# Kernel optimization log

Hardware: AMD Instinct MI355X
Metric: run time of the kernel (lower is better)

Reference implementation:

```python
import jax, jax.numpy as jnp
import numpy as np

D_MODEL = 1536
D_STATE = 96
D_CONV = 4
EXPAND = 2
COND_DIM = 1536
D_INNER = D_MODEL * EXPAND
DT_RANK = max(D_MODEL // 16, 1)
EPS = 1e-6


def setup_inputs() -> dict:
    key = jax.random.key(0)
    ks = jax.random.split(key, 12)
    B, L = 2, 2048
    s = 0.02
    x = jax.random.normal(ks[0], (B, L, D_MODEL), dtype=jnp.float32)
    t_cond = jax.random.normal(ks[1], (B, 1, COND_DIM), dtype=jnp.float32)
    cond_w = s * jax.random.normal(ks[2], (COND_DIM, 3 * D_MODEL), dtype=jnp.float32)
    cond_b = jnp.zeros((3 * D_MODEL,), dtype=jnp.float32).at[2 * D_MODEL:].set(2.0)
    in_w = s * jax.random.normal(ks[3], (D_MODEL, 2 * D_INNER), dtype=jnp.float32)
    conv_w = s * jax.random.normal(ks[4], (D_INNER, 1, D_CONV), dtype=jnp.float32)  # depthwise [O,I/g,K]
    conv_b = s * jax.random.normal(ks[5], (D_INNER,), dtype=jnp.float32)
    xproj_w = s * jax.random.normal(ks[6], (D_INNER, DT_RANK + 2 * D_STATE), dtype=jnp.float32)
    dt_w = s * jax.random.normal(ks[7], (DT_RANK, D_INNER), dtype=jnp.float32)
    dt_b = s * jax.random.normal(ks[8], (D_INNER,), dtype=jnp.float32)
    A_log = jnp.log(jnp.broadcast_to(jnp.arange(1, D_STATE + 1, dtype=jnp.float32)[None, :], (D_INNER, D_STATE)))
    D_param = jnp.ones((D_INNER,), dtype=jnp.float32)
    out_w = s * jax.random.normal(ks[9], (D_INNER, D_MODEL), dtype=jnp.float32)
    return {"x": x, "t_cond": t_cond, "cond_w": cond_w, "cond_b": cond_b,
            "in_w": in_w, "conv_w": conv_w, "conv_b": conv_b, "xproj_w": xproj_w,
            "dt_w": dt_w, "dt_b": dt_b, "A_log": A_log, "D_param": D_param, "out_w": out_w}


def _forward(x, t_cond, cond_w, cond_b, in_w, conv_w, conv_b, xproj_w, dt_w, dt_b, A_log, D_param, out_w):
    residual = x
    B, L, _ = x.shape
    # AdaRMSNorm
    rms = jax.lax.rsqrt(jnp.mean(x * x, axis=-1, keepdims=True) + EPS)
    xn = x * rms
    cond = t_cond @ cond_w + cond_b  # [B,1,3*D_MODEL]
    scale, shift, gate = jnp.split(cond, 3, axis=-1)
    xm = jax.nn.sigmoid(gate) * (xn * (1.0 + scale) + shift)
    # in_proj and split
    xz = xm @ in_w  # [B,L,2*D_INNER]
    x_main, z = xz[..., :D_INNER], xz[..., D_INNER:]
    # causal depthwise conv1d (torch pads both sides then slices [:L] -> left pad only)
    xc = jnp.swapaxes(x_main, 1, 2)  # [B,D_INNER,L]
    xc = jax.lax.conv_general_dilated(xc, conv_w, window_strides=(1,),
                                      padding=[(D_CONV - 1, 0)],
                                      feature_group_count=D_INNER,
                                      dimension_numbers=("NCH", "OIH", "NCH"))
    xc = xc + conv_b[None, :, None]
    x_main = jax.nn.silu(jnp.swapaxes(xc, 1, 2))  # [B,L,D_INNER]
    # SSM parameters
    A = -jnp.exp(A_log)  # [D_INNER,D_STATE]
    x_dbl = x_main @ xproj_w
    dt_raw = x_dbl[..., :DT_RANK]
    B_ssm = x_dbl[..., DT_RANK:DT_RANK + D_STATE]
    C_ssm = x_dbl[..., DT_RANK + D_STATE:]
    dt = jax.nn.softplus(dt_raw @ dt_w + dt_b)  # [B,L,D_INNER]
    # selective scan over time (avoids materializing [B,L,D_INNER,D_STATE])
    def step(state, inp):
        dt_t, B_t, C_t, x_t = inp  # [B,Di],[B,Ds],[B,Ds],[B,Di]
        dA = jnp.exp(dt_t[:, :, None] * A)  # [B,Di,Ds]
        state = state * dA + (dt_t * x_t)[:, :, None] * B_t[:, None, :]
        y_t = jnp.einsum("bdn,bn->bd", state, C_t)
        return state, y_t

    state0 = jnp.zeros((B, D_INNER, D_STATE), dtype=x.dtype)
    xs = (jnp.swapaxes(dt, 0, 1), jnp.swapaxes(B_ssm, 0, 1),
          jnp.swapaxes(C_ssm, 0, 1), jnp.swapaxes(x_main, 0, 1))
    _, y = jax.lax.scan(step, state0, xs)  # y: [L,B,D_INNER]
    y = jnp.swapaxes(y, 0, 1)
    y = y + x_main * D_param[None, None, :]
    y = y * jax.nn.silu(z)
    return residual + y @ out_w


def reference(x, t_cond, cond_w, cond_b, in_w, conv_w, conv_b, xproj_w, dt_w, dt_b, A_log, D_param, out_w):
    return _forward(x, t_cond, cond_w, cond_b, in_w, conv_w, conv_b, xproj_w, dt_w, dt_b, A_log, D_param, out_w)
```

## Files before the change

### kernel.cpp

```cpp
#include <hip/hip_runtime.h>
#include <hip/hip_bf16.h>
#include <cstdint>
#include <cstddef>

#define L_SEQ 2048
#define NBATCH 2
#define M_TOT 4096
#define DM 1536
#define DI 3072
#define DS 96
#define DTR 96
#define XDBL_LD 384

typedef __attribute__((ext_vector_type(8))) short bf16x8;
typedef __attribute__((ext_vector_type(4))) float f32x4;
typedef __hip_bfloat16 bf16;

__device__ __forceinline__ float bf2f(bf16 h) { return __bfloat162float(h); }
__device__ __forceinline__ bf16 f2bf(float f) { return __float2bfloat16(f); }

__device__ __forceinline__ void gload_lds16(const void* g, void* lds) {
  __builtin_amdgcn_global_load_lds(
      (const __attribute__((address_space(1))) void*)g,
      (__attribute__((address_space(3))) void*)lds, 16, 0, 0);
}

__global__ void cond_kernel(const float* __restrict__ t_cond,
                            const float* __restrict__ cond_w,
                            const float* __restrict__ cond_b,
                            float* __restrict__ cond_mod) {
  int idx = blockIdx.x * 256 + threadIdx.x;
  int b = idx / 4608;
  int j = idx - b * 4608;
  const float* tc = t_cond + b * DM;
  float a0 = 0.f, a1 = 0.f, a2 = 0.f, a3 = 0.f;
#pragma unroll 4
  for (int k = 0; k < DM; k += 4) {
    a0 += tc[k + 0] * cond_w[(size_t)(k + 0) * 4608 + j];
    a1 += tc[k + 1] * cond_w[(size_t)(k + 1) * 4608 + j];
    a2 += tc[k + 2] * cond_w[(size_t)(k + 2) * 4608 + j];
    a3 += tc[k + 3] * cond_w[(size_t)(k + 3) * 4608 + j];
  }
  float acc = cond_b[j] + ((a0 + a1) + (a2 + a3));
  if (j >= 2 * DM) acc = 1.f / (1.f + __expf(-acc));
  cond_mod[idx] = acc;
}

__global__ __launch_bounds__(256)
void rmsmod_kernel(const float* __restrict__ x,
                   const float* __restrict__ cond_mod,
                   bf16* __restrict__ xm) {
  int row = blockIdx.x;
  int b = row >> 11;
  const float* xr = x + (size_t)row * DM;
  const float* cm = cond_mod + b * 4608;
  float v[6];
  float ss = 0.f;
#pragma unroll
  for (int i = 0; i < 6; ++i) {
    v[i] = xr[threadIdx.x + i * 256];
    ss += v[i] * v[i];
  }
#pragma unroll
  for (int m = 32; m >= 1; m >>= 1) ss += __shfl_xor(ss, m);
  __shared__ float red[4];
  if ((threadIdx.x & 63) == 0) red[threadIdx.x >> 6] = ss;
  __syncthreads();
  float tot = red[0] + red[1] + red[2] + red[3];
  float rms = rsqrtf(tot * (1.f / (float)DM) + 1e-6f);
#pragma unroll
  for (int i = 0; i < 6; ++i) {
    int c = threadIdx.x + i * 256;
    float val = cm[3072 + c] * (v[i] * rms * (1.f + cm[c]) + cm[1536 + c]);
    xm[(size_t)row * DM + c] = f2bf(val);
  }
}

__global__ __launch_bounds__(256)
void transpose_cast(const float* __restrict__ src, bf16* __restrict__ dst,
                    int K, int N, int Ndst) {
  __shared__ float tile[64][65];
  int n0 = blockIdx.x * 64, k0 = blockIdx.y * 64;
#pragma unroll
  for (int i = 0; i < 16; ++i) {
    int idx = threadIdx.x + i * 256;
    int kk = idx >> 6, nn = idx & 63;
    float v = 0.f;
    if (k0 + kk < K && n0 + nn < N) v = src[(size_t)(k0 + kk) * N + (n0 + nn)];
    tile[kk][nn] = v;
  }
  __syncthreads();
#pragma unroll
  for (int i = 0; i < 16; ++i) {
    int idx = threadIdx.x + i * 256;
    int nn = idx >> 6, kk = idx & 63;
    if (n0 + nn < Ndst && k0 + kk < K)
      dst[(size_t)(n0 + nn) * K + (k0 + kk)] = f2bf(tile[kk][nn]);
  }
}

__global__ __launch_bounds__(256)
void tbf16_kernel(const bf16* __restrict__ src, int srcLD, int colOff,
                  bf16* __restrict__ dst) {
  __shared__ unsigned short tile[64][72];
  int bz = blockIdx.x / (48 * 32);
  int rem = blockIdx.x % (48 * 32);
  int td = rem % 48, tl = rem / 48;
  int l0 = tl * 64, d0 = td * 64;
  const bf16* s0 = src + ((size_t)bz * L_SEQ + l0) * srcLD + colOff + d0;
#pragma unroll
  for (int it = 0; it < 2; ++it) {
    int t = threadIdx.x + it * 256;
    int r = t >> 3, c8 = t & 7;
    bf16x8 v = *(const bf16x8*)(s0 + (size_t)r * srcLD + c8 * 8);
    *(bf16x8*)&tile[r][c8 * 8] = v;
  }
  __syncthreads();
  int dd = threadIdx.x & 63;
  int l16 = threadIdx.x >> 6;
  bf16* dp = dst + ((size_t)bz * DI + d0 + dd) * L_SEQ + l0 + l16 * 16;
  bf16x8 v0, v1;
#pragma unroll
  for (int j = 0; j < 8; ++j) v0[j] = (short)tile[l16 * 16 + j][dd];
#pragma unroll
  for (int j = 0; j < 8; ++j) v1[j] = (short)tile[l16 * 16 + 8 + j][dd];
  *(bf16x8*)dp = v0;
  *(bf16x8*)(dp + 8) = v1;
}

__global__ __launch_bounds__(256)
void conv_kernel(const bf16* __restrict__ xz, const float* __restrict__ conv_w,
                 const float* __restrict__ conv_b, bf16* __restrict__ xconv) {
  int idx = blockIdx.x * 256 + threadIdx.x;
  int d = idx % DI;
  int row = idx / DI;
  int l = row & (L_SEQ - 1);
  float4 w4 = *(const float4*)(conv_w + d * 4);
  const float wv[4] = {w4.x, w4.y, w4.z, w4.w};
  float acc = conv_b[d];
#pragma unroll
  for (int t = 0; t < 4; ++t) {
    int ll = l - 3 + t;
    if (ll >= 0) acc += bf2f(xz[(size_t)(row - 3 + t) * 6144 + d]) * wv[t];
  }
  xconv[idx] = f2bf(acc / (1.f + __expf(-acc)));
}

__global__ __launch_bounds__(256)
void dtraw_cast(const float* __restrict__ xdbl, bf16* __restrict__ dtraw) {
  int idx = blockIdx.x * 256 + threadIdx.x;
  int r = idx / DTR, c = idx - r * DTR;
  dtraw[idx] = f2bf(xdbl[(size_t)r * XDBL_LD + c]);
}

template <int EPI>
__global__ __launch_bounds__(256)
void gemm128(const bf16* __restrict__ A, int lda, const bf16* __restrict__ Bt,
             int ldb, void* __restrict__ C, int ldc,
             const float* __restrict__ extra, int nTilesN, int K) {
  __shared__ __align__(16) bf16 As[128 * 32];
  __shared__ __align__(16) bf16 Bs[128 * 32];
  const int tid = threadIdx.x;
  const int lane = tid & 63;
  const int wid = tid >> 6;
  const int bm = (blockIdx.x / nTilesN) * 128;
  const int bn = (blockIdx.x % nTilesN) * 128;
  const int wr = wid >> 1, wc = wid & 1;
  f32x4 acc[4][4] = {};
  for (int k0 = 0; k0 < K; k0 += 32) {
#pragma unroll
    for (int it = 0; it < 2; ++it) {
      int chunk = (wid * 2 + it) * 64 + lane;
      int row = chunk >> 2;
      int ke = (chunk & 3) * 8;
      gload_lds16(A + (size_t)(bm + row) * lda + (k0 + ke),
                  (char*)As + (size_t)(wid * 2 + it) * 1024);
      gload_lds16(Bt + (size_t)(bn + row) * ldb + (k0 + ke),
                  (char*)Bs + (size_t)(wid * 2 + it) * 1024);
    }
    __syncthreads();
    bf16x8 af[4], bfr[4];
#pragma unroll
    for (int m = 0; m < 4; ++m)
      af[m] = *(const bf16x8*)(As + (wr * 64 + m * 16 + (lane & 15)) * 32 +
                               (lane >> 4) * 8);
#pragma unroll
    for (int n = 0; n < 4; ++n)
      bfr[n] = *(const bf16x8*)(Bs + (wc * 64 + n * 16 + (lane & 15)) * 32 +
                                (lane >> 4) * 8);
#pragma unroll
    for (int m = 0; m < 4; ++m)
#pragma unroll
      for (int n = 0; n < 4; ++n)
        acc[m][n] =
            __builtin_amdgcn_mfma_f32_16x16x32_bf16(af[m], bfr[n], acc[m][n], 0, 0, 0);
    __syncthreads();
  }
  const int r0 = bm + wr * 64 + (lane >> 4) * 4;
  const int c0 = bn + wc * 64 + (lane & 15);
#pragma unroll
  for (int m = 0; m < 4; ++m) {
#pragma unroll
    for (int n = 0; n < 4; ++n) {
      int c = c0 + n * 16;
#pragma unroll
      for (int j = 0; j < 4; ++j) {
        int r = r0 + m * 16 + j;
        size_t off = (size_t)r * ldc + c;
        float v = acc[m][n][j];
        if constexpr (EPI == 0) {
          ((bf16*)C)[off] = f2bf(v);
        } else if constexpr (EPI == 1) {
          ((float*)C)[off] = v;
        } else if constexpr (EPI == 2) {
          float t = v + extra[c];
          ((bf16*)C)[off] = f2bf(t > 20.f ? t : log1pf(__expf(t)));
        } else {
          ((float*)C)[off] = v + extra[off];
        }
      }
    }
  }
}

__global__ __launch_bounds__(128)
void scan2_kernel(const bf16* __restrict__ dtT, const bf16* __restrict__ xcT,
                  const bf16* __restrict__ zT, const float* __restrict__ xdbl,
                  const float* __restrict__ A_log, const float* __restrict__ Dp,
                  bf16* __restrict__ yy) {
  const int tid = threadIdx.x;
  const int g = tid & 15;
  const int cl = tid >> 4;
  const int CH = blockIdx.x * 8 + cl;
  const int b = CH >= DI ? 1 : 0;
  const int d = CH - b * DI;
  const int n0 = g * 6;

  float a[6];
#pragma unroll
  for (int j = 0; j < 6; ++j) a[j] = -__expf(A_log[(size_t)d * DS + n0 + j]);
  const float Dd = Dp[d];
  float s[6] = {0.f, 0.f, 0.f, 0.f, 0.f, 0.f};

  const bf16* dtp = dtT + (size_t)CH * L_SEQ;
  const bf16* xcp = xcT + (size_t)CH * L_SEQ;
  const bf16* zp = zT + (size_t)CH * L_SEQ;
  const float* xb = xdbl + (size_t)b * L_SEQ * XDBL_LD;
  bf16* yp = yy + (size_t)b * L_SEQ * DI + d;

  float2 B2[2][3], C2[2][3];
#pragma unroll
  for (int sl = 0; sl < 2; ++sl) {
    const float2* pb = (const float2*)(xb + (size_t)sl * XDBL_LD + DTR + n0);
    const float2* pc = (const float2*)(xb + (size_t)sl * XDBL_LD + DTR + DS + n0);
#pragma unroll
    for (int j = 0; j < 3; ++j) {
      B2[sl][j] = pb[j];
      C2[sl][j] = pc[j];
    }
  }
  bf16x8 dt8 = *(const bf16x8*)dtp;
  bf16x8 xc8 = *(const bf16x8*)xcp;
  bf16x8 z8 = *(const bf16x8*)zp;

  for (int l0 = 0; l0 < L_SEQ; l0 += 8) {
    int ln = (l0 + 8) & (L_SEQ - 1);
    bf16x8 dt8n = *(const bf16x8*)(dtp + ln);
    bf16x8 xc8n = *(const bf16x8*)(xcp + ln);
    bf16x8 z8n = *(const bf16x8*)(zp + ln);
#pragma unroll
    for (int i = 0; i < 8; ++i) {
      int l = l0 + i;
      float dtv = __uint_as_float(((unsigned)(unsigned short)dt8[i]) << 16);
      float xv = __uint_as_float(((unsigned)(unsigned short)xc8[i]) << 16);
      float du = dtv * xv;
      float pj = 0.f;
#pragma unroll
      for (int j = 0; j < 6; ++j) {
        float Bj = (j & 1) ? B2[i & 1][j >> 1].y : B2[i & 1][j >> 1].x;
        float Cj = (j & 1) ? C2[i & 1][j >> 1].y : C2[i & 1][j >> 1].x;
        s[j] = s[j] * __expf(dtv * a[j]) + du * Bj;
        pj += s[j] * Cj;
      }
      int lp = l + 2;
      if (lp > L_SEQ - 1) lp = L_SEQ - 1;
      {
        const float2* pb = (const float2*)(xb + (size_t)lp * XDBL_LD + DTR + n0);
        const float2* pc =
            (const float2*)(xb + (size_t)lp * XDBL_LD + DTR + DS + n0);
#pragma unroll
        for (int j = 0; j < 3; ++j) {
          B2[i & 1][j] = pb[j];
          C2[i & 1][j] = pc[j];
        }
      }
      pj += __shfl_xor(pj, 8);
      pj += __shfl_xor(pj, 4);
      pj += __shfl_xor(pj, 2);
      pj += __shfl_xor(pj, 1);
      if (g == 0) {
        float zv = __uint_as_float(((unsigned)(unsigned short)z8[i]) << 16);
        float y = pj + xv * Dd;
        yp[(size_t)l * DI] = f2bf(y * (zv / (1.f + __expf(-zv))));
      }
    }
    dt8 = dt8n;
    xc8 = xc8n;
    z8 = z8n;
  }
}

extern "C" void kernel_launch(void* const* d_in, const int* in_sizes, int n_in,
                              void* d_out, int out_size, void* d_ws,
                              size_t ws_size, hipStream_t stream) {
  const float* x = (const float*)d_in[0];
  const float* t_cond = (const float*)d_in[1];
  const float* cond_w = (const float*)d_in[2];
  const float* cond_b = (const float*)d_in[3];
  const float* in_w = (const float*)d_in[4];
  const float* conv_w = (const float*)d_in[5];
  const float* conv_b = (const float*)d_in[6];
  const float* xproj_w = (const float*)d_in[7];
  const float* dt_w = (const float*)d_in[8];
  const float* dt_b = (const float*)d_in[9];
  const float* A_log = (const float*)d_in[10];
  const float* D_p = (const float*)d_in[11];
  const float* out_w = (const float*)d_in[12];
  float* out = (float*)d_out;

  char* ws = (char*)d_ws;
  size_t off = 0;
  auto alloc = [&](size_t bytes) {
    void* p = ws + off;
    off += (bytes + 255) & ~(size_t)255;
    return p;
  };
  float* cond_mod = (float*)alloc(2 * 4608 * 4);
  char* regionA = (char*)alloc(31457280);
  bf16* xm = (bf16*)regionA;
  bf16* in_w_t = (bf16*)(regionA + (size_t)M_TOT * DM * 2);
  bf16* xcT = (bf16*)regionA;
  bf16* xproj_t = (bf16*)alloc((size_t)XDBL_LD * DI * 2);
  bf16* dtw_t = (bf16*)alloc((size_t)DI * DTR * 2);
  bf16* outw_t = (bf16*)alloc((size_t)DM * DI * 2);
  char* xzR = (char*)alloc((size_t)M_TOT * 6144 * 2);
  bf16* xz = (bf16*)xzR;
  bf16* dtT = (bf16*)xzR;
  bf16* dtraw = (bf16*)(xzR + 25165824);
  bf16* yy = (bf16*)(xzR + 25952256);
  char* xcR = (char*)alloc((size_t)M_TOT * DI * 2);
  bf16* xconv = (bf16*)xcR;
  bf16* zT = (bf16*)xcR;
  float* xdbl = (float*)alloc((size_t)M_TOT * XDBL_LD * 4);
  bf16* dtbuf = (bf16*)alloc((size_t)M_TOT * DI * 2);

  cond_kernel<<<36, 256, 0, stream>>>(t_cond, cond_w, cond_b, cond_mod);
  rmsmod_kernel<<<M_TOT, 256, 0, stream>>>(x, cond_mod, xm);
  transpose_cast<<<dim3(96, 24), 256, 0, stream>>>(in_w, in_w_t, 1536, 6144, 6144);
  transpose_cast<<<dim3(6, 48), 256, 0, stream>>>(xproj_w, xproj_t, 3072, 288, 384);
  transpose_cast<<<dim3(48, 2), 256, 0, stream>>>(dt_w, dtw_t, 96, 3072, 3072);
  transpose_cast<<<dim3(24, 48), 256, 0, stream>>>(out_w, outw_t, 3072, 1536, 1536);
  gemm128<0><<<32 * 48, 256, 0, stream>>>(xm, DM, in_w_t, DM, xz, 6144,
                                          nullptr, 48, DM);
  conv_kernel<<<(M_TOT * DI) / 256, 256, 0, stream>>>(xz, conv_w, conv_b, xconv);
  gemm128<1><<<32 * 3, 256, 0, stream>>>(xconv, DI, xproj_t, DI, xdbl, XDBL_LD,
                                         nullptr, 3, DI);
  tbf16_kernel<<<2 * 48 * 32, 256, 0, stream>>>(xconv, DI, 0, xcT);
  tbf16_kernel<<<2 * 48 * 32, 256, 0, stream>>>(xz, 6144, DI, zT);
  dtraw_cast<<<(M_TOT * DTR) / 256, 256, 0, stream>>>(xdbl, dtraw);
  gemm128<2><<<32 * 24, 256, 0, stream>>>(dtraw, DTR, dtw_t, DTR, dtbuf, DI,
                                          dt_b, 24, DTR);
  tbf16_kernel<<<2 * 48 * 32, 256, 0, stream>>>(dtbuf, DI, 0, dtT);
  scan2_kernel<<<768, 128, 0, stream>>>(dtT, xcT, zT, xdbl, A_log, D_p, yy);
  gemm128<3><<<32 * 12, 256, 0, stream>>>(yy, DI, outw_t, DI, out, DM, x, 12,
                                          DI);
}
```

Measured before the change: 1.486 ms.

## Split selective scan into chunked two-pass scan with cross-chunk state combine

```diff
diff --git a/kernel.cpp b/kernel.cpp
--- a/kernel.cpp
+++ b/kernel.cpp
@@ -12,12 +12,26 @@
 #define DTR 96
 #define XDBL_LD 384
 
+#define NCHUNK 8
+#define CLEN 256
+#define SUBS 16
+#define NSUB (CLEN / SUBS)
+
 typedef __attribute__((ext_vector_type(8))) short bf16x8;
 typedef __attribute__((ext_vector_type(4))) float f32x4;
 typedef __hip_bfloat16 bf16;
 
 __device__ __forceinline__ float bf2f(bf16 h) { return __bfloat162float(h); }
 __device__ __forceinline__ bf16 f2bf(float f) { return __float2bfloat16(f); }
+__device__ __forceinline__ float bfbits(short h) {
+  return __uint_as_float(((unsigned)(unsigned short)h) << 16);
+}
+#if __has_builtin(__builtin_amdgcn_exp2f)
+__device__ __forceinline__ float fexp2(float x) { return __builtin_amdgcn_exp2f(x); }
+#else
+__device__ __forceinline__ float fexp2(float x) { return exp2f(x); }
+#endif
+#define LOG2E 1.44269504f
 
 __device__ __forceinline__ void gload_lds16(const void* g, void* lds) {
   __builtin_amdgcn_global_load_lds(
@@ -223,90 +237,169 @@
   }
 }
 
-__global__ __launch_bounds__(128)
-void scan2_kernel(const bf16* __restrict__ dtT, const bf16* __restrict__ xcT,
-                  const bf16* __restrict__ zT, const float* __restrict__ xdbl,
-                  const float* __restrict__ A_log, const float* __restrict__ Dp,
-                  bf16* __restrict__ yy) {
+template <int PASS>
+__global__ __launch_bounds__(256)
+void scan_pass(const bf16* __restrict__ dtT, const bf16* __restrict__ xcT,
+               const bf16* __restrict__ zT, const float* __restrict__ xdbl,
+               const float* __restrict__ A_log, const float* __restrict__ Dp,
+               float* __restrict__ q, float* __restrict__ sumdt,
+               bf16* __restrict__ yy) {
+  constexpr int SW = (PASS == 1) ? 96 : 192;
+  constexpr int NF4 = SUBS * SW / 4;
+  __shared__ float bcs[2][SUBS][SW];
   const int tid = threadIdx.x;
   const int g = tid & 15;
   const int cl = tid >> 4;
-  const int CH = blockIdx.x * 8 + cl;
-  const int b = CH >= DI ? 1 : 0;
-  const int d = CH - b * DI;
+  const int ch = blockIdx.x * 16 + cl;
+  const int c = blockIdx.y;
+  const int b = ch >= DI ? 1 : 0;
+  const int d = ch - b * DI;
   const int n0 = g * 6;
-
-  float a[6];
-#pragma unroll
-  for (int j = 0; j < 6; ++j) a[j] = -__expf(A_log[(size_t)d * DS + n0 + j]);
-  const float Dd = Dp[d];
+  const int l0 = c * CLEN;
+
+  float a2[6];
+#pragma unroll
+  for (int j = 0; j < 6; ++j)
+    a2[j] = -__expf(A_log[(size_t)d * DS + n0 + j]) * LOG2E;
+
+  float s[6];
+  if (PASS == 1) {
+#pragma unroll
+    for (int j = 0; j < 6; ++j) s[j] = 0.f;
+  } else {
+#pragma unroll
+    for (int j = 0; j < 6; ++j)
+      s[j] = q[((size_t)ch * NCHUNK + c) * DS + n0 + j];
+  }
+  const float Dd = (PASS == 2) ? Dp[d] : 0.f;
+  float sdt = 0.f;
+
+  const bf16* dtp = dtT + (size_t)ch * L_SEQ + l0;
+  const bf16* xcp = xcT + (size_t)ch * L_SEQ + l0;
+  const bf16* zp = zT + (size_t)ch * L_SEQ + l0;
+  const float* xb = xdbl + ((size_t)b * L_SEQ + l0) * XDBL_LD + DTR;
+  bf16* yp = yy + ((size_t)b * L_SEQ + l0) * DI + d;
+
+  float4 rg[3];
+#pragma unroll
+  for (int k = 0; k < 3; ++k) {
+    int f = tid + k * 256;
+    if (f < NF4) {
+      int row = f / (SW / 4), c4 = f % (SW / 4);
+      rg[k] = *(const float4*)(xb + (size_t)row * XDBL_LD + c4 * 4);
+    }
+  }
+#pragma unroll
+  for (int k = 0; k < 3; ++k) {
+    int f = tid + k * 256;
+    if (f < NF4) ((float4*)&bcs[0][0][0])[f] = rg[k];
+  }
+  __syncthreads();
+
+  int cur = 0;
+  for (int sc = 0; sc < NSUB; ++sc) {
+    if (sc < NSUB - 1) {
+#pragma unroll
+      for (int k = 0; k < 3; ++k) {
+        int f = tid + k * 256;
+        if (f < NF4) {
+          int row = f / (SW / 4), c4 = f % (SW / 4);
+          rg[k] = *(const float4*)(xb + (size_t)((sc + 1) * SUBS + row) * XDBL_LD +
+                                   c4 * 4);
+        }
+      }
+    }
+    bf16x8 dt8a = *(const bf16x8*)(dtp + sc * SUBS);
+    bf16x8 dt8b = *(const bf16x8*)(dtp + sc * SUBS + 8);
+    bf16x8 xc8a = *(const bf16x8*)(xcp + sc * SUBS);
+    bf16x8 xc8b = *(const bf16x8*)(xcp + sc * SUBS + 8);
+    bf16x8 z8a = {}, z8b = {};
+    if (PASS == 2) {
+      z8a = *(const bf16x8*)(zp + sc * SUBS);
+      z8b = *(const bf16x8*)(zp + sc * SUBS + 8);
+    }
+#pragma unroll
+    for (int i = 0; i < SUBS; ++i) {
+      float dtv = bfbits(i < 8 ? dt8a[i] : dt8b[i - 8]);
+      float xv = bfbits(i < 8 ? xc8a[i] : xc8b[i - 8]);
+      float du = dtv * xv;
+      if (PASS == 1) sdt += dtv;
+      const float* brow = &bcs[cur][i][0];
+      float pj = 0.f;
+      float2 Bv[3], Cv[3];
+#pragma unroll
+      for (int j3 = 0; j3 < 3; ++j3) {
+        Bv[j3] = *(const float2*)(brow + n0 + 2 * j3);
+        if (PASS == 2) Cv[j3] = *(const float2*)(brow + 96 + n0 + 2 * j3);
+      }
+#pragma unroll
+      for (int j = 0; j < 6; ++j) {
+        float e = fexp2(dtv * a2[j]);
+        float Bj = (j & 1) ? Bv[j >> 1].y : Bv[j >> 1].x;
+        s[j] = s[j] * e + du * Bj;
+        if (PASS == 2) {
+          float Cj = (j & 1) ? Cv[j >> 1].y : Cv[j >> 1].x;
+          pj += s[j] * Cj;
+        }
+      }
+      if (PASS == 2) {
+        pj += __shfl_xor(pj, 8);
+        pj += __shfl_xor(pj, 4);
+        pj += __shfl_xor(pj, 2);
+        pj += __shfl_xor(pj, 1);
+        if (g == 0) {
+          float zv = bfbits(i < 8 ? z8a[i] : z8b[i - 8]);
+          float y = pj + xv * Dd;
+          yp[(size_t)(sc * SUBS + i) * DI] = f2bf(y * (zv / (1.f + __expf(-zv))));
+        }
+      }
+    }
+    if (sc < NSUB - 1) {
+#pragma unroll
+      for (int k = 0; k < 3; ++k) {
+        int f = tid + k * 256;
+        if (f < NF4) ((float4*)&bcs[cur ^ 1][0][0])[f] = rg[k];
+      }
+      __syncthreads();
+      cur ^= 1;
+    }
+  }
+
+  if (PASS == 1) {
+    float* qp = q + ((size_t)ch * NCHUNK + c) * DS + n0;
+#pragma unroll
+    for (int j = 0; j < 6; ++j) qp[j] = s[j];
+    if (g == 0) sumdt[ch * NCHUNK + c] = sdt;
+  }
+}
+
+__global__ __launch_bounds__(256)
+void scan_combine(const float* __restrict__ A_log, float* __restrict__ q,
+                  const float* __restrict__ sumdt) {
+  int idx = blockIdx.x * 256 + threadIdx.x;
+  int ch = idx >> 4, g = idx & 15;
+  int b = ch >= DI ? 1 : 0;
+  int d = ch - b * DI;
+  int n0 = g * 6;
+  float a2[6];
+#pragma unroll
+  for (int j = 0; j < 6; ++j)
+    a2[j] = -__expf(A_log[(size_t)d * DS + n0 + j]) * LOG2E;
   float s[6] = {0.f, 0.f, 0.f, 0.f, 0.f, 0.f};
-
-  const bf16* dtp = dtT + (size_t)CH * L_SEQ;
-  const bf16* xcp = xcT + (size_t)CH * L_SEQ;
-  const bf16* zp = zT + (size_t)CH * L_SEQ;
-  const float* xb = xdbl + (size_t)b * L_SEQ * XDBL_LD;
-  bf16* yp = yy + (size_t)b * L_SEQ * DI + d;
-
-  float2 B2[2][3], C2[2][3];
-#pragma unroll
-  for (int sl = 0; sl < 2; ++sl) {
-    const float2* pb = (const float2*)(xb + (size_t)sl * XDBL_LD + DTR + n0);
-    const float2* pc = (const float2*)(xb + (size_t)sl * XDBL_LD + DTR + DS + n0);
-#pragma unroll
-    for (int j = 0; j < 3; ++j) {
-      B2[sl][j] = pb[j];
-      C2[sl][j] = pc[j];
-    }
-  }
-  bf16x8 dt8 = *(const bf16x8*)dtp;
-  bf16x8 xc8 = *(const bf16x8*)xcp;
-  bf16x8 z8 = *(const bf16x8*)zp;
-
-  for (int l0 = 0; l0 < L_SEQ; l0 += 8) {
-    int ln = (l0 + 8) & (L_SEQ - 1);
-    bf16x8 dt8n = *(const bf16x8*)(dtp + ln);
-    bf16x8 xc8n = *(const bf16x8*)(xcp + ln);
-    bf16x8 z8n = *(const bf16x8*)(zp + ln);
-#pragma unroll
-    for (int i = 0; i < 8; ++i) {
-      int l = l0 + i;
-      float dtv = __uint_as_float(((unsigned)(unsigned short)dt8[i]) << 16);
-      float xv = __uint_as_float(((unsigned)(unsigned short)xc8[i]) << 16);
-      float du = dtv * xv;
-      float pj = 0.f;
-#pragma unroll
-      for (int j = 0; j < 6; ++j) {
-        float Bj = (j & 1) ? B2[i & 1][j >> 1].y : B2[i & 1][j >> 1].x;
-        float Cj = (j & 1) ? C2[i & 1][j >> 1].y : C2[i & 1][j >> 1].x;
-        s[j] = s[j] * __expf(dtv * a[j]) + du * Bj;
-        pj += s[j] * Cj;
-      }
-      int lp = l + 2;
-      if (lp > L_SEQ - 1) lp = L_SEQ - 1;
-      {
-        const float2* pb = (const float2*)(xb + (size_t)lp * XDBL_LD + DTR + n0);
-        const float2* pc =
-            (const float2*)(xb + (size_t)lp * XDBL_LD + DTR + DS + n0);
-#pragma unroll
-        for (int j = 0; j < 3; ++j) {
-          B2[i & 1][j] = pb[j];
-          C2[i & 1][j] = pc[j];
-        }
-      }
-      pj += __shfl_xor(pj, 8);
-      pj += __shfl_xor(pj, 4);
-      pj += __shfl_xor(pj, 2);
-      pj += __shfl_xor(pj, 1);
-      if (g == 0) {
-        float zv = __uint_as_float(((unsigned)(unsigned short)z8[i]) << 16);
-        float y = pj + xv * Dd;
-        yp[(size_t)l * DI] = f2bf(y * (zv / (1.f + __expf(-zv))));
-      }
-    }
-    dt8 = dt8n;
-    xc8 = xc8n;
-    z8 = z8n;
+  for (int c = 0; c < NCHUNK; ++c) {
+    float sd = sumdt[ch * NCHUNK + c];
+    float* qp = q + ((size_t)ch * NCHUNK + c) * DS + n0;
+    float qc[6];
+#pragma unroll
+    for (int j = 0; j < 6; ++j) {
+      qc[j] = qp[j];
+      qp[j] = s[j];
+    }
+#pragma unroll
+    for (int j = 0; j < 6; ++j) {
+      float P = fexp2(a2[j] * sd);
+      s[j] = P * s[j] + qc[j];
+    }
   }
 }
 
@@ -352,7 +445,10 @@
   bf16* xconv = (bf16*)xcR;
   bf16* zT = (bf16*)xcR;
   float* xdbl = (float*)alloc((size_t)M_TOT * XDBL_LD * 4);
-  bf16* dtbuf = (bf16*)alloc((size_t)M_TOT * DI * 2);
+  char* dtR = (char*)alloc((size_t)M_TOT * DI * 2);
+  bf16* dtbuf = (bf16*)dtR;
+  float* qbuf = (float*)dtR;
+  float* sumdt = (float*)alloc((size_t)2 * DI * NCHUNK * 4);
 
   cond_kernel<<<36, 256, 0, stream>>>(t_cond, cond_w, cond_b, cond_mod);
   rmsmod_kernel<<<M_TOT, 256, 0, stream>>>(x, cond_mod, xm);
@@ -371,7 +467,11 @@
   gemm128<2><<<32 * 24, 256, 0, stream>>>(dtraw, DTR, dtw_t, DTR, dtbuf, DI,
                                           dt_b, 24, DTR);
   tbf16_kernel<<<2 * 48 * 32, 256, 0, stream>>>(dtbuf, DI, 0, dtT);
-  scan2_kernel<<<768, 128, 0, stream>>>(dtT, xcT, zT, xdbl, A_log, D_p, yy);
+  scan_pass<1><<<dim3(384, NCHUNK), 256, 0, stream>>>(
+      dtT, xcT, zT, xdbl, A_log, D_p, qbuf, sumdt, yy);
+  scan_combine<<<384, 256, 0, stream>>>(A_log, qbuf, sumdt);
+  scan_pass<2><<<dim3(384, NCHUNK), 256, 0, stream>>>(
+      dtT, xcT, zT, xdbl, A_log, D_p, qbuf, sumdt, yy);
   gemm128<3><<<32 * 12, 256, 0, stream>>>(yy, DI, outw_t, DI, out, DM, x, 12,
                                           DI);
 }
```

Result: faster. 1.231 ms (-17.1%).
